# Optimization experiments

Measured on AMD Instinct MI355X. Metric: run time of the kernel, lower is better.

## Reference

```python
import jax, jax.numpy as jnp
import numpy as np

NUM_HEADS = 8
ATTN_LEN = 5


def setup_inputs() -> dict:
    rng = jax.random.key(0)
    ks = jax.random.split(rng, 10)
    B, T, D = 2, 4096, 1024
    H, HD = NUM_HEADS, D // NUM_HEADS
    n = lambda k, shape, scale=1.0: jax.random.normal(k, shape, jnp.float32) * scale
    return {
        "query": n(ks[0], (B, T, D)),
        "key": n(ks[1], (B, T, D)),
        "value": n(ks[2], (B, T, D)),
        "Wq": n(ks[3], (D, D), 0.02),
        "bq": jnp.zeros((D,), jnp.float32),
        "Wk": n(ks[4], (D, D), 0.02),
        "bk": jnp.zeros((D,), jnp.float32),
        "Wv": n(ks[5], (D, D), 0.02),
        "bv": jnp.zeros((D,), jnp.float32),
        "Er": n(ks[6], (H, HD, ATTN_LEN)),
        "layer": 1,
    }


def _forward(query, key, value, Wq, bq, Wk, bk, Wv, bv, Er, layer):
    B, T, D = query.shape
    H = NUM_HEADS
    HD = D // H
    dil = 2 ** layer
    pad = dil * (ATTN_LEN // 2)
    Tp = T + 2 * pad

    # torch nn.Linear: y = x @ W^T + b ; reshape to [B, H, T, HD]
    q = (query @ Wq.T + bq).reshape(B, T, H, HD).transpose(0, 2, 1, 3)
    k = (key @ Wk.T + bk).reshape(B, T, H, HD).transpose(0, 2, 1, 3)
    v = (value @ Wv.T + bv).reshape(B, T, H, HD).transpose(0, 2, 1, 3)

    # head-group source mapping + shifts (note k head 7 reuses k head 6, per source)
    src_k = jnp.array([0, 1, 2, 3, 4, 5, 6, 6])
    src_v = jnp.array([0, 1, 2, 3, 4, 5, 6, 7])
    shifts = jnp.array([0, 0, 0, 0, -2, -1, 1, 2])

    # kv_roll equivalence: window slot j at time t for shift s reads
    # padded[(t + (s + j) * dil) mod Tp]  (torch.roll wraparound included)
    t_idx = jnp.arange(T)
    j_idx = jnp.arange(ATTN_LEN)
    idx = (t_idx[None, :, None] + (shifts[:, None, None] + j_idx[None, None, :]) * dil) % Tp  # [H,T,L]

    def windows(x, src):
        xp = jnp.pad(x, ((0, 0), (0, 0), (pad, pad), (0, 0)))[:, src]  # [B,H,Tp,HD]
        g = jnp.take_along_axis(xp, idx.reshape(1, H, T * ATTN_LEN, 1), axis=2)
        return g.reshape(B, H, T, ATTN_LEN, HD)

    kw = windows(k, src_k)  # [B,H,T,L,HD]
    vw = windows(v, src_v)

    qk = jnp.einsum('bhtd,bhtjd->bhtj', q, kw)            # [B,H,T,L]
    mask = jnp.where(qk == 0.0, -jnp.inf, 0.0)            # zero dot product => padding
    qer = jnp.einsum('bhtd,hdj->bhtj', q, Er)             # relative positional bias
    attn = jax.nn.softmax((qk + qer) / np.sqrt(HD).astype(np.float32) + mask, axis=-1)
    out = jnp.einsum('bhtj,bhtjd->bhtd', attn, vw)        # [B,H,T,HD]
    out = out.transpose(0, 2, 1, 3).reshape(B, T, D)
    return out, attn[:, :, :, None, :]                     # attn shaped [B,H,T,1,L] like torch


def reference(query, key, value, Wq, bq, Wk, bk, Wv, bv, Er, layer):
    return _forward(query, key, value, Wq, bq, Wk, bk, Wv, bv, Er, layer)
```

## Files before the change

### kernel.cpp

```cpp
#include <hip/hip_runtime.h>
#include <hip/hip_bf16.h>

constexpr int B_ = 2, T_ = 4096, D_ = 1024, H_ = 8, HD_ = 128, L_ = 5;
constexpr int M_ = B_ * T_;
constexpr int K_ = D_;
constexpr int N_ = D_;
constexpr int TB_ = 64;
constexpr int NSMAX_ = 72;

typedef __attribute__((ext_vector_type(8))) __bf16 bf16x8;
typedef __attribute__((ext_vector_type(4))) __bf16 bf16x4;
typedef __attribute__((ext_vector_type(4))) float f32x4;

__device__ __constant__ int c_srck[8]  = {0, 1, 2, 3, 4, 5, 6, 6};
__device__ __constant__ int c_shift[8] = {0, 0, 0, 0, -2, -1, 1, 2};

__device__ __forceinline__ void gload_lds16(const void* g, void* l) {
    __builtin_amdgcn_global_load_lds(
        (__attribute__((address_space(1))) void*)g,
        (__attribute__((address_space(3))) void*)l, 16, 0, 0);
}

__global__ __launch_bounds__(256) void cvt_kernel(
    const float* __restrict__ q,  const float* __restrict__ k,  const float* __restrict__ v,
    const float* __restrict__ wq, const float* __restrict__ wk, const float* __restrict__ wv,
    __hip_bfloat16* __restrict__ qb,  __hip_bfloat16* __restrict__ kb,  __hip_bfloat16* __restrict__ vb,
    __hip_bfloat16* __restrict__ wqb, __hip_bfloat16* __restrict__ wkb, __hip_bfloat16* __restrict__ wvb)
{
    const int y = blockIdx.y;
    const float* src;
    __hip_bfloat16* dst;
    size_t base;
    if (blockIdx.x < 2048) {
        src = (y == 0) ? q : (y == 1) ? k : v;
        dst = (y == 0) ? qb : (y == 1) ? kb : vb;
        base = (size_t)blockIdx.x * 4096;
    } else {
        src = (y == 0) ? wq : (y == 1) ? wk : wv;
        dst = (y == 0) ? wqb : (y == 1) ? wkb : wvb;
        base = (size_t)(blockIdx.x - 2048) * 4096;
    }
    const int tid = threadIdx.x;
#pragma unroll
    for (int c = 0; c < 4; ++c) {
        const size_t idx = base + (size_t)c * 1024 + (size_t)tid * 4;
        f32x4 a = *(const f32x4*)(const void*)(src + idx);
        bf16x4 o;
#pragma unroll
        for (int e = 0; e < 4; ++e) o[e] = (__bf16)a[e];
        *(bf16x4*)(void*)(dst + idx) = o;
    }
}

__global__ __launch_bounds__(256) void qkv_gemm_bf16(
    const __hip_bfloat16* __restrict__ qb,
    const __hip_bfloat16* __restrict__ kb,
    const __hip_bfloat16* __restrict__ vb,
    const __hip_bfloat16* __restrict__ wqb,
    const __hip_bfloat16* __restrict__ wkb,
    const __hip_bfloat16* __restrict__ wvb,
    const float* __restrict__ bq,
    const float* __restrict__ bk,
    const float* __restrict__ bv,
    __hip_bfloat16* __restrict__ qout,
    __hip_bfloat16* __restrict__ kout,
    __hip_bfloat16* __restrict__ vout)
{
    const int z = blockIdx.z;
    const __hip_bfloat16* A = (z == 0) ? qb  : (z == 1) ? kb  : vb;
    const __hip_bfloat16* W = (z == 0) ? wqb : (z == 1) ? wkb : wvb;
    const float* bias       = (z == 0) ? bq  : (z == 1) ? bk  : bv;
    __hip_bfloat16* C       = (z == 0) ? qout : (z == 1) ? kout : vout;

    __shared__ __align__(16) __hip_bfloat16 As[128 * 32];
    __shared__ __align__(16) __hip_bfloat16 Bs[128 * 32];

    const int tid  = threadIdx.x;
    const int wave = tid >> 6;
    const int lane = tid & 63;
    const int m0 = blockIdx.x * 128;
    const int n0 = blockIdx.y * 128;
    const int wm = (wave >> 1) * 64;
    const int wn = (wave & 1) * 64;

    f32x4 acc[4][4];
#pragma unroll
    for (int i = 0; i < 4; ++i)
#pragma unroll
        for (int j = 0; j < 4; ++j)
            acc[i][j] = (f32x4){0.f, 0.f, 0.f, 0.f};

    const int srow = lane >> 2;
    const int scol = (lane & 3) * 8;
    const int fr = lane & 15;
    const int fk = (lane >> 4) * 8;

    for (int k0 = 0; k0 < K_; k0 += 32) {
#pragma unroll
        for (int r = 0; r < 2; ++r) {
            const int issue = wave + r * 4;
            const int row = issue * 16 + srow;
            gload_lds16(A + (size_t)(m0 + row) * K_ + k0 + scol,
                        (void*)(As + issue * 512));
            gload_lds16(W + (size_t)(n0 + row) * K_ + k0 + scol,
                        (void*)(Bs + issue * 512));
        }
        __syncthreads();

        bf16x8 af[4], bf[4];
#pragma unroll
        for (int i = 0; i < 4; ++i) {
            af[i] = *(const bf16x8*)(const void*)(As + (wm + i * 16 + fr) * 32 + fk);
            bf[i] = *(const bf16x8*)(const void*)(Bs + (wn + i * 16 + fr) * 32 + fk);
        }
#pragma unroll
        for (int i = 0; i < 4; ++i)
#pragma unroll
            for (int j = 0; j < 4; ++j)
                acc[i][j] = __builtin_amdgcn_mfma_f32_16x16x32_bf16(
                    af[i], bf[j], acc[i][j], 0, 0, 0);
        __syncthreads();
    }

    const int col_l = lane & 15;
    const int row_l = (lane >> 4) * 4;
#pragma unroll
    for (int j = 0; j < 4; ++j) {
        const int n = n0 + wn + j * 16 + col_l;
        const float bval = bias[n];
#pragma unroll
        for (int i = 0; i < 4; ++i) {
            const int m = m0 + wm + i * 16 + row_l;
#pragma unroll
            for (int r = 0; r < 4; ++r)
                C[(size_t)(m + r) * N_ + n] = __float2bfloat16(acc[i][j][r] + bval);
        }
    }
}

__global__ __launch_bounds__(256) void qkv_gemm_f32(
    const float* __restrict__ query,
    const float* __restrict__ key,
    const float* __restrict__ value,
    const float* __restrict__ Wq,
    const float* __restrict__ bq,
    const float* __restrict__ Wk,
    const float* __restrict__ bk,
    const float* __restrict__ Wv,
    const float* __restrict__ bv,
    __hip_bfloat16* __restrict__ qout,
    __hip_bfloat16* __restrict__ kout,
    __hip_bfloat16* __restrict__ vout)
{
    const int z = blockIdx.z;
    const float* A    = (z == 0) ? query : (z == 1) ? key : value;
    const float* W    = (z == 0) ? Wq    : (z == 1) ? Wk  : Wv;
    const float* bias = (z == 0) ? bq    : (z == 1) ? bk  : bv;
    __hip_bfloat16* C = (z == 0) ? qout  : (z == 1) ? kout : vout;

    __shared__ __align__(16) float As[128 * 32];
    __shared__ __align__(16) float Bs[128 * 32];

    const int tid  = threadIdx.x;
    const int wave = tid >> 6;
    const int lane = tid & 63;
    const int m0 = blockIdx.x * 128;
    const int n0 = blockIdx.y * 128;
    const int wm = (wave >> 1) * 64;
    const int wn = (wave & 1) * 64;

    f32x4 acc[4][4];
#pragma unroll
    for (int i = 0; i < 4; ++i)
#pragma unroll
        for (int j = 0; j < 4; ++j)
            acc[i][j] = (f32x4){0.f, 0.f, 0.f, 0.f};

    const int srow = lane >> 3;
    const int lcg  = (lane & 7) ^ srow;
    const int gcol = lcg * 4;

    const int fr  = lane & 15;
    const int r7  = fr & 7;
    const int cgA = (lane >> 4) * 2;
    const int pcg0 = (cgA)     ^ r7;
    const int pcg1 = (cgA ^ 1) ^ r7;

    for (int k0 = 0; k0 < K_; k0 += 32) {
#pragma unroll
        for (int r = 0; r < 4; ++r) {
            const int issue = wave + r * 4;
            const int row = issue * 8 + srow;
            gload_lds16(A + (size_t)(m0 + row) * K_ + k0 + gcol,
                        (void*)(As + issue * 256));
            gload_lds16(W + (size_t)(n0 + row) * K_ + k0 + gcol,
                        (void*)(Bs + issue * 256));
        }
        __syncthreads();

        bf16x8 af[4], bf[4];
#pragma unroll
        for (int i = 0; i < 4; ++i) {
            const float* ap = As + (wm + i * 16 + fr) * 32;
            f32x4 a0 = *(const f32x4*)(const void*)(ap + pcg0 * 4);
            f32x4 a1 = *(const f32x4*)(const void*)(ap + pcg1 * 4);
            const float* bp = Bs + (wn + i * 16 + fr) * 32;
            f32x4 b0 = *(const f32x4*)(const void*)(bp + pcg0 * 4);
            f32x4 b1 = *(const f32x4*)(const void*)(bp + pcg1 * 4);
#pragma unroll
            for (int e = 0; e < 4; ++e) {
                af[i][e]     = (__bf16)a0[e];
                af[i][e + 4] = (__bf16)a1[e];
                bf[i][e]     = (__bf16)b0[e];
                bf[i][e + 4] = (__bf16)b1[e];
            }
        }
#pragma unroll
        for (int i = 0; i < 4; ++i)
#pragma unroll
            for (int j = 0; j < 4; ++j)
                acc[i][j] = __builtin_amdgcn_mfma_f32_16x16x32_bf16(
                    af[i], bf[j], acc[i][j], 0, 0, 0);
        __syncthreads();
    }

    const int col_l = lane & 15;
    const int row_l = (lane >> 4) * 4;
#pragma unroll
    for (int j = 0; j < 4; ++j) {
        const int n = n0 + wn + j * 16 + col_l;
        const float bval = bias[n];
#pragma unroll
        for (int i = 0; i < 4; ++i) {
            const int m = m0 + wm + i * 16 + row_l;
#pragma unroll
            for (int r = 0; r < 4; ++r)
                C[(size_t)(m + r) * N_ + n] = __float2bfloat16(acc[i][j][r] + bval);
        }
    }
}

__global__ __launch_bounds__(256) void attn_kernel(
    const __hip_bfloat16* __restrict__ qp,
    const __hip_bfloat16* __restrict__ kp,
    const __hip_bfloat16* __restrict__ vp,
    const float* __restrict__ Er,
    const int* __restrict__ layer_p,
    float* __restrict__ out,
    float* __restrict__ attn_out)
{
    const int dil = 1 << (*layer_p);
    int NS = TB_ + 4 * dil;
    if (NS > NSMAX_) NS = NSMAX_;

    const int tid = threadIdx.x;
    const int t0 = blockIdx.x * TB_;
    const int h  = blockIdx.y;
    const int b  = blockIdx.z;
    const int shift = c_shift[h];
    const int srck  = c_srck[h];
    const int off_lo = (shift - 2) * dil;

    __shared__ __align__(16) __hip_bfloat16 Ks[NSMAX_ * 128];
    __shared__ __align__(16) __hip_bfloat16 Vs[NSMAX_ * 128];
    __shared__ __align__(16) float ErT[5][128];

    for (int i = tid; i < 640; i += 256) {
        const int d = i / 5, j = i - d * 5;
        ErT[j][d] = Er[(size_t)h * 640 + i];
    }

    const int sr = tid >> 4;
    const int sc = tid & 15;
    for (int i0 = 0; i0 < NS; i0 += 16) {
        const int i = i0 + sr;
        if (i < NS) {
            int r = t0 + off_lo + i;
            r = (r < 0) ? 0 : (r >= T_ ? T_ - 1 : r);
            bf16x8 kv8 = *(const bf16x8*)(const void*)(
                kp + (size_t)(b * T_ + r) * D_ + srck * HD_ + sc * 8);
            bf16x8 vv8 = *(const bf16x8*)(const void*)(
                vp + (size_t)(b * T_ + r) * D_ + h * HD_ + sc * 8);
            const int pc = sc ^ (i & 3);
            *(bf16x8*)(void*)(Ks + i * 128 + pc * 8) = kv8;
            *(bf16x8*)(void*)(Vs + i * 128 + pc * 8) = vv8;
        }
    }
    __syncthreads();

    const int lr = tid >> 2;
    const int ld = tid & 3;
    const int t  = t0 + lr;
    const size_t qoff = (size_t)(b * T_ + t) * D_ + h * HD_ + ld * 32;

    float qf[32];
#pragma unroll
    for (int c = 0; c < 4; ++c) {
        bf16x8 qv = *(const bf16x8*)(const void*)(qp + qoff + c * 8);
#pragma unroll
        for (int e = 0; e < 8; ++e) qf[c * 8 + e] = (float)qv[e];
    }

    float lg[5];
    bool  valid[5];
#pragma unroll
    for (int j = 0; j < 5; ++j) {
        const int i = lr + j * dil;
        const int orig = t + (shift + j - 2) * dil;
        valid[j] = (orig >= 0) && (orig < T_);

        float s = 0.f;
#pragma unroll
        for (int c = 0; c < 4; ++c) {
            const int pc = (ld * 4 + c) ^ (i & 3);
            bf16x8 kk = *(const bf16x8*)(const void*)(Ks + i * 128 + pc * 8);
#pragma unroll
            for (int e = 0; e < 8; ++e) s += qf[c * 8 + e] * (float)kk[e];
        }
        if (!valid[j]) s = 0.f;
#pragma unroll
        for (int c = 0; c < 8; ++c) {
            f32x4 ev = *(const f32x4*)(const void*)(&ErT[j][ld * 32 + c * 4]);
#pragma unroll
            for (int e = 0; e < 4; ++e) s += qf[c * 4 + e] * ev[e];
        }
        s += __shfl_xor(s, 1, 4);
        s += __shfl_xor(s, 2, 4);
        lg[j] = valid[j] ? s * 0.08838834764831845f : -INFINITY;
    }

    float mx = lg[0];
#pragma unroll
    for (int j = 1; j < 5; ++j) mx = fmaxf(mx, lg[j]);
    float w[5], sum = 0.f;
#pragma unroll
    for (int j = 0; j < 5; ++j) {
        w[j] = valid[j] ? __expf(lg[j] - mx) : 0.f;
        sum += w[j];
    }
    const float inv = 1.f / sum;
#pragma unroll
    for (int j = 0; j < 5; ++j) w[j] *= inv;

    float o[32];
#pragma unroll
    for (int m = 0; m < 32; ++m) o[m] = 0.f;
#pragma unroll
    for (int j = 0; j < 5; ++j) {
        const int i = lr + j * dil;
#pragma unroll
        for (int c = 0; c < 4; ++c) {
            const int pc = (ld * 4 + c) ^ (i & 3);
            bf16x8 vv = *(const bf16x8*)(const void*)(Vs + i * 128 + pc * 8);
#pragma unroll
            for (int e = 0; e < 8; ++e) o[c * 8 + e] += w[j] * (float)vv[e];
        }
    }

#pragma unroll
    for (int c = 0; c < 8; ++c) {
        f32x4 ov = (f32x4){o[c * 4], o[c * 4 + 1], o[c * 4 + 2], o[c * 4 + 3]};
        *(f32x4*)(void*)(out + qoff + c * 4) = ov;
    }

    const size_t abase = ((size_t)(b * H_ + h) * T_ + t) * L_;
    attn_out[abase + ld] = w[ld];
    if (ld == 0) attn_out[abase + 4] = w[4];
}

extern "C" void kernel_launch(void* const* d_in, const int* in_sizes, int n_in,
                              void* d_out, int out_size, void* d_ws, size_t ws_size,
                              hipStream_t stream) {
    const float* query = (const float*)d_in[0];
    const float* key   = (const float*)d_in[1];
    const float* value = (const float*)d_in[2];
    const float* Wq    = (const float*)d_in[3];
    const float* bq    = (const float*)d_in[4];
    const float* Wk    = (const float*)d_in[5];
    const float* bk    = (const float*)d_in[6];
    const float* Wv    = (const float*)d_in[7];
    const float* bv    = (const float*)d_in[8];
    const float* Er    = (const float*)d_in[9];
    const int*   layer = (const int*)d_in[10];

    float* out  = (float*)d_out;
    float* attn = out + (size_t)B_ * T_ * D_;

    const size_t SA = (size_t)M_ * K_;
    const size_t SW = (size_t)N_ * K_;
    const size_t SP = (size_t)M_ * N_;
    const size_t need = (3 * SA + 3 * SW + 3 * SP) * sizeof(__hip_bfloat16);

    char* ws = (char*)d_ws;
    if (ws_size >= need) {
        __hip_bfloat16* qb  = (__hip_bfloat16*)ws;
        __hip_bfloat16* kb  = qb + SA;
        __hip_bfloat16* vb  = kb + SA;
        __hip_bfloat16* wqb = vb + SA;
        __hip_bfloat16* wkb = wqb + SW;
        __hip_bfloat16* wvb = wkb + SW;
        __hip_bfloat16* qp  = wvb + SW;
        __hip_bfloat16* kp  = qp + SP;
        __hip_bfloat16* vp  = kp + SP;

        cvt_kernel<<<dim3(2304, 3), 256, 0, stream>>>(
            query, key, value, Wq, Wk, Wv, qb, kb, vb, wqb, wkb, wvb);

        qkv_gemm_bf16<<<dim3(M_ / 128, N_ / 128, 3), 256, 0, stream>>>(
            qb, kb, vb, wqb, wkb, wvb, bq, bk, bv, qp, kp, vp);

        attn_kernel<<<dim3(T_ / TB_, H_, B_), 256, 0, stream>>>(
            qp, kp, vp, Er, layer, out, attn);
    } else {
        __hip_bfloat16* qp = (__hip_bfloat16*)ws;
        __hip_bfloat16* kp = qp + SP;
        __hip_bfloat16* vp = kp + SP;

        qkv_gemm_f32<<<dim3(M_ / 128, N_ / 128, 3), 256, 0, stream>>>(
            query, key, value, Wq, bq, Wk, bk, Wv, bv, qp, kp, vp);

        attn_kernel<<<dim3(T_ / TB_, H_, B_), 256, 0, stream>>>(
            qp, kp, vp, Er, layer, out, attn);
    }
}
```

Measured before the change: 255.4 us.

## Retile attention to 32-row blocks with 8 lanes per row and widen conversion

The attention kernel now handles 32 timesteps per block with 8 threads per row, each covering 16 head dims. This halves per-thread registers, doubles the number of blocks and uses a 3-step shuffle reduction. K/V staging loads are issued in a batch before the LDS stores, with an XOR swizzle over 8 chunks, and the Er table row is padded to avoid bank conflicts. The f32-to-bf16 conversion kernel now handles 8 elements per thread with 16-byte stores and issues all its loads up front, using half as many blocks. The aim is more parallelism and memory-level overlap, at the cost of more halo reloading per block and more shuffle work.

```diff
diff --git a/kernel.cpp b/kernel.cpp
--- a/kernel.cpp
+++ b/kernel.cpp
@@ -5,11 +5,10 @@
 constexpr int M_ = B_ * T_;
 constexpr int K_ = D_;
 constexpr int N_ = D_;
-constexpr int TB_ = 64;
-constexpr int NSMAX_ = 72;
+constexpr int TB_ = 32;
+constexpr int NSMAX_ = 48;
 
 typedef __attribute__((ext_vector_type(8))) __bf16 bf16x8;
-typedef __attribute__((ext_vector_type(4))) __bf16 bf16x4;
 typedef __attribute__((ext_vector_type(4))) float f32x4;
 
 __device__ __constant__ int c_srck[8]  = {0, 1, 2, 3, 4, 5, 6, 6};
@@ -31,24 +30,33 @@
     const float* src;
     __hip_bfloat16* dst;
     size_t base;
-    if (blockIdx.x < 2048) {
+    if (blockIdx.x < 1024) {
         src = (y == 0) ? q : (y == 1) ? k : v;
         dst = (y == 0) ? qb : (y == 1) ? kb : vb;
-        base = (size_t)blockIdx.x * 4096;
+        base = (size_t)blockIdx.x * 8192;
     } else {
         src = (y == 0) ? wq : (y == 1) ? wk : wv;
         dst = (y == 0) ? wqb : (y == 1) ? wkb : wvb;
-        base = (size_t)(blockIdx.x - 2048) * 4096;
+        base = (size_t)(blockIdx.x - 1024) * 8192;
     }
     const int tid = threadIdx.x;
-#pragma unroll
-    for (int c = 0; c < 4; ++c) {
-        const size_t idx = base + (size_t)c * 1024 + (size_t)tid * 4;
-        f32x4 a = *(const f32x4*)(const void*)(src + idx);
-        bf16x4 o;
-#pragma unroll
-        for (int e = 0; e < 4; ++e) o[e] = (__bf16)a[e];
-        *(bf16x4*)(void*)(dst + idx) = o;
+    f32x4 a[8];
+#pragma unroll
+    for (int it = 0; it < 4; ++it) {
+        const size_t idx = base + (size_t)it * 2048 + (size_t)tid * 8;
+        a[2 * it]     = *(const f32x4*)(const void*)(src + idx);
+        a[2 * it + 1] = *(const f32x4*)(const void*)(src + idx + 4);
+    }
+#pragma unroll
+    for (int it = 0; it < 4; ++it) {
+        const size_t idx = base + (size_t)it * 2048 + (size_t)tid * 8;
+        bf16x8 o;
+#pragma unroll
+        for (int e = 0; e < 4; ++e) {
+            o[e]     = (__bf16)a[2 * it][e];
+            o[e + 4] = (__bf16)a[2 * it + 1][e];
+        }
+        *(bf16x8*)(void*)(dst + idx) = o;
     }
 }
 
@@ -263,7 +271,7 @@
 
     __shared__ __align__(16) __hip_bfloat16 Ks[NSMAX_ * 128];
     __shared__ __align__(16) __hip_bfloat16 Vs[NSMAX_ * 128];
-    __shared__ __align__(16) float ErT[5][128];
+    __shared__ __align__(16) float ErT[5][132];
 
     for (int i = tid; i < 640; i += 256) {
         const int d = i / 5, j = i - d * 5;
@@ -272,30 +280,34 @@
 
     const int sr = tid >> 4;
     const int sc = tid & 15;
-    for (int i0 = 0; i0 < NS; i0 += 16) {
-        const int i = i0 + sr;
-        if (i < NS) {
-            int r = t0 + off_lo + i;
-            r = (r < 0) ? 0 : (r >= T_ ? T_ - 1 : r);
-            bf16x8 kv8 = *(const bf16x8*)(const void*)(
-                kp + (size_t)(b * T_ + r) * D_ + srck * HD_ + sc * 8);
-            bf16x8 vv8 = *(const bf16x8*)(const void*)(
-                vp + (size_t)(b * T_ + r) * D_ + h * HD_ + sc * 8);
-            const int pc = sc ^ (i & 3);
-            *(bf16x8*)(void*)(Ks + i * 128 + pc * 8) = kv8;
-            *(bf16x8*)(void*)(Vs + i * 128 + pc * 8) = vv8;
-        }
+    bf16x8 kbuf[3], vbuf[3];
+#pragma unroll
+    for (int p = 0; p < 3; ++p) {
+        const int i = p * 16 + sr;
+        int r = t0 + off_lo + i;
+        r = (r < 0) ? 0 : (r >= T_ ? T_ - 1 : r);
+        kbuf[p] = *(const bf16x8*)(const void*)(
+            kp + (size_t)(b * T_ + r) * D_ + srck * HD_ + sc * 8);
+        vbuf[p] = *(const bf16x8*)(const void*)(
+            vp + (size_t)(b * T_ + r) * D_ + h * HD_ + sc * 8);
+    }
+#pragma unroll
+    for (int p = 0; p < 3; ++p) {
+        const int i = p * 16 + sr;
+        const int pc = sc ^ (i & 7);
+        *(bf16x8*)(void*)(Ks + i * 128 + pc * 8) = kbuf[p];
+        *(bf16x8*)(void*)(Vs + i * 128 + pc * 8) = vbuf[p];
     }
     __syncthreads();
 
-    const int lr = tid >> 2;
-    const int ld = tid & 3;
+    const int lr = tid >> 3;
+    const int ld = tid & 7;
     const int t  = t0 + lr;
-    const size_t qoff = (size_t)(b * T_ + t) * D_ + h * HD_ + ld * 32;
-
-    float qf[32];
-#pragma unroll
-    for (int c = 0; c < 4; ++c) {
+    const size_t qoff = (size_t)(b * T_ + t) * D_ + h * HD_ + ld * 16;
+
+    float qf[16];
+#pragma unroll
+    for (int c = 0; c < 2; ++c) {
         bf16x8 qv = *(const bf16x8*)(const void*)(qp + qoff + c * 8);
 #pragma unroll
         for (int e = 0; e < 8; ++e) qf[c * 8 + e] = (float)qv[e];
@@ -311,21 +323,22 @@
 
         float s = 0.f;
 #pragma unroll
+        for (int c = 0; c < 2; ++c) {
+            const int pc = (ld * 2 + c) ^ (i & 7);
+            bf16x8 kk = *(const bf16x8*)(const void*)(Ks + i * 128 + pc * 8);
+#pragma unroll
+            for (int e = 0; e < 8; ++e) s += qf[c * 8 + e] * (float)kk[e];
+        }
+        if (!valid[j]) s = 0.f;
+#pragma unroll
         for (int c = 0; c < 4; ++c) {
-            const int pc = (ld * 4 + c) ^ (i & 3);
-            bf16x8 kk = *(const bf16x8*)(const void*)(Ks + i * 128 + pc * 8);
-#pragma unroll
-            for (int e = 0; e < 8; ++e) s += qf[c * 8 + e] * (float)kk[e];
-        }
-        if (!valid[j]) s = 0.f;
-#pragma unroll
-        for (int c = 0; c < 8; ++c) {
-            f32x4 ev = *(const f32x4*)(const void*)(&ErT[j][ld * 32 + c * 4]);
+            f32x4 ev = *(const f32x4*)(const void*)(&ErT[j][ld * 16 + c * 4]);
 #pragma unroll
             for (int e = 0; e < 4; ++e) s += qf[c * 4 + e] * ev[e];
         }
-        s += __shfl_xor(s, 1, 4);
-        s += __shfl_xor(s, 2, 4);
+        s += __shfl_xor(s, 1, 8);
+        s += __shfl_xor(s, 2, 8);
+        s += __shfl_xor(s, 4, 8);
         lg[j] = valid[j] ? s * 0.08838834764831845f : -INFINITY;
     }
 
@@ -342,15 +355,15 @@
 #pragma unroll
     for (int j = 0; j < 5; ++j) w[j] *= inv;
 
-    float o[32];
-#pragma unroll
-    for (int m = 0; m < 32; ++m) o[m] = 0.f;
+    float o[16];
+#pragma unroll
+    for (int m = 0; m < 16; ++m) o[m] = 0.f;
 #pragma unroll
     for (int j = 0; j < 5; ++j) {
         const int i = lr + j * dil;
 #pragma unroll
-        for (int c = 0; c < 4; ++c) {
-            const int pc = (ld * 4 + c) ^ (i & 3);
+        for (int c = 0; c < 2; ++c) {
+            const int pc = (ld * 2 + c) ^ (i & 7);
             bf16x8 vv = *(const bf16x8*)(const void*)(Vs + i * 128 + pc * 8);
 #pragma unroll
             for (int e = 0; e < 8; ++e) o[c * 8 + e] += w[j] * (float)vv[e];
@@ -358,14 +371,13 @@
     }
 
 #pragma unroll
-    for (int c = 0; c < 8; ++c) {
+    for (int c = 0; c < 4; ++c) {
         f32x4 ov = (f32x4){o[c * 4], o[c * 4 + 1], o[c * 4 + 2], o[c * 4 + 3]};
         *(f32x4*)(void*)(out + qoff + c * 4) = ov;
     }
 
     const size_t abase = ((size_t)(b * H_ + h) * T_ + t) * L_;
-    attn_out[abase + ld] = w[ld];
-    if (ld == 0) attn_out[abase + 4] = w[4];
+    if (ld < 5) attn_out[abase + ld] = w[ld];
 }
 
 extern "C" void kernel_launch(void* const* d_in, const int* in_sizes, int n_in,
@@ -403,7 +415,7 @@
         __hip_bfloat16* kp  = qp + SP;
         __hip_bfloat16* vp  = kp + SP;
 
-        cvt_kernel<<<dim3(2304, 3), 256, 0, stream>>>(
+        cvt_kernel<<<dim3(1152, 3), 256, 0, stream>>>(
             query, key, value, Wq, Wk, Wv, qb, kb, vb, wqb, wkb, wvb);
 
         qkv_gemm_bf16<<<dim3(M_ / 128, N_ / 128, 3), 256, 0, stream>>>(
```

New measurement: 257.1 us. No clear change (+0.6%).
